# Kernel optimization log

Hardware: AMD Instinct MI355X
Metric: run time of the kernel (lower is better)

The kernel has to match this reference:

```python
import jax, jax.numpy as jnp
import numpy as np

DIM = 256
N_PATCHES = 2048
N_HEADS = 8
BATCH = 2


def setup_inputs() -> dict:
    key = jax.random.key(0)
    ks = jax.random.split(key, 8)
    d = DIM
    s = d ** -0.5
    return {
        "x": jax.random.normal(ks[0], (BATCH, N_PATCHES, d), dtype=jnp.float32),
        # weights stored (in_features, out_features) so y = x @ W + b
        "W_qk": jax.random.normal(ks[1], (d, 2 * d), dtype=jnp.float32) * s,
        "W_v": jax.random.normal(ks[2], (d, d), dtype=jnp.float32) * s,
        "W_proj": jax.random.normal(ks[3], (d, d), dtype=jnp.float32) * s,
        "b_proj": jnp.zeros((d,), dtype=jnp.float32),
        "W_pos": jax.random.normal(ks[4], (2, N_HEADS), dtype=jnp.float32) * 0.5,
        "b_pos": jnp.zeros((N_HEADS,), dtype=jnp.float32),
        "gating": jnp.ones((N_HEADS,), dtype=jnp.float32),
    }


def reference(x, W_qk, W_v, W_proj, b_proj, W_pos, b_pos, gating):
    B, N, C = x.shape
    H = gating.shape[0]
    Dh = C // H
    scale = Dh ** -0.5

    # content attention: q @ k^T softmax
    qk = (x @ W_qk).reshape(B, N, 2, H, Dh)
    q = jnp.transpose(qk[:, :, 0], (0, 2, 1, 3))  # [B,H,N,Dh]
    k = jnp.transpose(qk[:, :, 1], (0, 2, 1, 3))
    patch_score = jax.nn.softmax(jnp.einsum("bhnd,bhmd->bhnm", q, k) * scale, axis=-1)

    # positional attention from relative indices (d, |d|) -> per-head score
    idx = jnp.arange(N, dtype=jnp.float32)
    rel = idx[:, None] - idx[None, :]                      # [N,N]
    rel_feat = jnp.stack([rel, jnp.abs(rel)], axis=-1)     # [N,N,2]
    pos = rel_feat @ W_pos + b_pos                         # [N,N,H]
    pos_score = jax.nn.softmax(jnp.transpose(pos, (2, 0, 1)), axis=-1)  # [H,N,N]

    g = jax.nn.sigmoid(gating)[None, :, None, None]        # [1,H,1,1]
    attn = (1.0 - g) * patch_score + g * pos_score[None]   # [B,H,N,N]
    attn = attn / jnp.sum(attn, axis=-1, keepdims=True)

    v = jnp.transpose((x @ W_v).reshape(B, N, H, Dh), (0, 2, 1, 3))  # [B,H,N,Dh]
    out = jnp.einsum("bhnm,bhmd->bhnd", attn, v)
    out = jnp.transpose(out, (0, 2, 1, 3)).reshape(B, N, C)
    return out @ W_proj + b_proj
```

## Files before the change

### kernel.cpp

```cpp
#include <hip/hip_runtime.h>
#include <hip/hip_bf16.h>

#define DIM 256
#define NP 2048
#define NH 8
#define BATCH 2
#define DH 32

typedef __attribute__((ext_vector_type(8))) short bshort8;
typedef __attribute__((ext_vector_type(4))) short bshort4;
typedef __attribute__((ext_vector_type(4))) float f32x4;

#define LOG2E 1.44269504f
#define QSCALE (0.17677669529663687f * LOG2E)

union U16B { uint4 u; bshort8 s8; __hip_bfloat16 h[8]; };
union U8B  { uint2 u; bshort4 s4; __hip_bfloat16 h[4]; };

__device__ __forceinline__ float fexp2(float x) { return __builtin_amdgcn_exp2f(x); }
__device__ __forceinline__ unsigned packbf(float hi, float lo) {
    return __builtin_amdgcn_perm(__float_as_uint(hi), __float_as_uint(lo), 0x07060302u);
}

__device__ __forceinline__ int lds_addr(int row, int colg) {
    return row * 256 + (((colg ^ (row & 7)) & 31) << 3);
}

__global__ __launch_bounds__(256) void prep_kernel(
    const float* __restrict__ Wqk,
    const float* __restrict__ Wv,
    const float* __restrict__ Wproj,
    __hip_bfloat16* __restrict__ WT) {
    const int t = threadIdx.x;
    const int blk = blockIdx.x;
    __shared__ float ts[64][65];
    const int ct = blk >> 2, k0 = (blk & 3) * 64;
    const int c0 = ct * 64;
    const float* src; int ldw, cs0; float scl = 1.0f;
    if (ct < 8)       { src = Wqk;   ldw = 512; cs0 = c0;      if (ct < 4) scl = QSCALE; }
    else if (ct < 12) { src = Wv;    ldw = 256; cs0 = c0 - 512; }
    else              { src = Wproj; ldw = 256; cs0 = c0 - 768; }
    const int cc = t & 63, tq = t >> 6;
#pragma unroll
    for (int j = 0; j < 16; j++) {
        int kk = tq * 16 + j;
        ts[kk][cc] = src[(size_t)(k0 + kk) * ldw + cs0 + cc];
    }
    __syncthreads();
    const int kk2 = t & 63;
#pragma unroll
    for (int j = 0; j < 16; j++) {
        int cc2 = tq * 16 + j;
        WT[(size_t)(c0 + cc2) * 256 + k0 + kk2] = __float2bfloat16(ts[kk2][cc2] * scl);
    }
}

__global__ __launch_bounds__(256) void qkv_mfma(
    const float* __restrict__ x,
    const __hip_bfloat16* __restrict__ WT,
    __hip_bfloat16* __restrict__ q,
    __hip_bfloat16* __restrict__ k,
    __hip_bfloat16* __restrict__ vF) {
    __shared__ __align__(16) __hip_bfloat16 As[64 * 256];
    __shared__ __align__(16) __hip_bfloat16 Bs[64 * 256];
    const int t = threadIdx.x, lane = t & 63, wvid = t >> 6;
    const int l15 = lane & 15, l4 = lane >> 4;
    const int m0 = blockIdx.x * 64;
    const int nb0 = blockIdx.y * 64;

#pragma unroll
    for (int j = 0; j < 8; j++) {
        const int flat = j * 2048 + t * 8;
        const int row = flat >> 8, colg = (flat >> 3) & 31;
        float4 f0 = *(const float4*)(x + (size_t)m0 * 256 + flat);
        float4 f1 = *(const float4*)(x + (size_t)m0 * 256 + flat + 4);
        U16B a;
        a.h[0] = __float2bfloat16(f0.x); a.h[1] = __float2bfloat16(f0.y);
        a.h[2] = __float2bfloat16(f0.z); a.h[3] = __float2bfloat16(f0.w);
        a.h[4] = __float2bfloat16(f1.x); a.h[5] = __float2bfloat16(f1.y);
        a.h[6] = __float2bfloat16(f1.z); a.h[7] = __float2bfloat16(f1.w);
        *(uint4*)&As[lds_addr(row, colg)] = a.u;
        *(uint4*)&Bs[lds_addr(row, colg)] = *(const uint4*)(WT + (size_t)nb0 * 256 + flat);
    }
    __syncthreads();

    f32x4 acc[4] = {{0.f,0.f,0.f,0.f},{0.f,0.f,0.f,0.f},{0.f,0.f,0.f,0.f},{0.f,0.f,0.f,0.f}};
#pragma unroll
    for (int kk = 0; kk < 8; kk++) {
        const int colg = kk * 4 + l4;
        U16B bw; bw.u = *(const uint4*)&Bs[lds_addr(wvid * 16 + l15, colg)];
#pragma unroll
        for (int mt = 0; mt < 4; mt++) {
            U16B ax; ax.u = *(const uint4*)&As[lds_addr(mt * 16 + l15, colg)];
            acc[mt] = __builtin_amdgcn_mfma_f32_16x16x32_bf16(ax.s8, bw.s8, acc[mt], 0, 0, 0);
        }
    }

    if (nb0 < 512) {
        __syncthreads();
        __hip_bfloat16* Tr = As;
#pragma unroll
        for (int mt = 0; mt < 4; mt++)
#pragma unroll
            for (int r = 0; r < 4; r++)
                Tr[(mt * 16 + l4 * 4 + r) * 72 + wvid * 16 + l15] = __float2bfloat16(acc[mt][r]);
        __syncthreads();
        const int hh = t >> 7, row = (t >> 1) & 63, part = t & 1;
        const bool isq = (nb0 < 256);
        const int cc = (isq ? nb0 : nb0 - 256) + hh * 32;
        const int hOut = cc >> 5;
        const int tok = m0 + row;
        const int b = tok >> 11, n = tok & (NP - 1);
        __hip_bfloat16* dst = (isq ? q : k) + ((size_t)(b * NH + hOut) * NP + n) * DH + part * 16;
        uint4 w0 = *(const uint4*)&Tr[row * 72 + hh * 32 + part * 16];
        uint4 w1 = *(const uint4*)&Tr[row * 72 + hh * 32 + part * 16 + 8];
        *(uint4*)dst = w0;
        *(uint4*)(dst + 8) = w1;
    } else {
        const int cbase = (nb0 - 512) + wvid * 16;
        const int h = cbase >> 5;
        const int vh = (cbase >> 4) & 1;
        const int b = m0 >> 11;
#pragma unroll
        for (int mt = 0; mt < 4; mt++) {
            const int kt = ((m0 & (NP - 1)) >> 4) + mt;
            U8B vv;
#pragma unroll
            for (int r = 0; r < 4; r++) vv.h[r] = __float2bfloat16(acc[mt][r]);
            *(uint2*)(vF + ((((size_t)((b * NH + h) * 128 + kt)) * 2 + vh) * 64 + lane) * 4) = vv.u;
        }
    }
}

__global__ __launch_bounds__(512, 4) void attn_kernel(
    const __hip_bfloat16* __restrict__ qg,
    const __hip_bfloat16* __restrict__ kg,
    const __hip_bfloat16* __restrict__ vF,
    const float* __restrict__ Wpos,
    const float* __restrict__ bpos,
    const float* __restrict__ gating,
    __hip_bfloat16* __restrict__ ao) {
    __shared__ __align__(16) __hip_bfloat16 Kt[2][2][64][40];
    __shared__ __align__(16) __hip_bfloat16 Vf[2][2][2048];
    __shared__ float cmb[4][2][32][16];
    __shared__ float cls[4][2][16];

    const int t = threadIdx.x;
    const int lane = t & 63, wvid = t >> 6;
    const int l15 = lane & 15, l4 = lane >> 4;
    const int qt = wvid & 3, kh = wvid >> 2;
    const int bh = blockIdx.x >> 5, qb = blockIdx.x & 31;
    const int h = bh & (NH - 1), b = bh >> 3;
    const int q0 = qb * 64 + qt * 16;
    const int myq = q0 + l15;

    const int st_ = t & 255;
    const int kstart = kh * 1024;
    const __hip_bfloat16* kptr = kg + (size_t)bh * NP * DH + (size_t)(kstart + (st_ >> 2)) * DH + (st_ & 3) * 8;
    const __hip_bfloat16* vptr = vF + (size_t)bh * 65536 + (size_t)kstart * 32 + st_ * 8;

    uint4 kreg = *(const uint4*)kptr;
    uint4 vreg = *(const uint4*)vptr;
    *(uint4*)&Kt[kh][0][st_ >> 2][(st_ & 3) * 8] = kreg;
    *(uint4*)&Vf[kh][0][st_ * 8] = vreg;

    const float w0 = Wpos[h] * LOG2E;
    const float w1 = Wpos[NH + h] * LOG2E;
    const float g = 1.0f / (1.0f + __expf(-gating[h]));
    const float nf = (float)myq;
    const float pmax = fmaxf(0.f, fmaxf((w0 + w1) * nf, (w1 - w0) * (2047.0f - nf)));
    const float npmax = -pmax;
    const float rA = fexp2(-(w0 + w1));
    const float rB = fexp2(w1 - w0);

    U16B qv;
    qv.u = *(const uint4*)(qg + ((size_t)bh * NP + myq) * DH + l4 * 8);

    __syncthreads();

    f32x4 os0 = {0.f,0.f,0.f,0.f}, os1 = {0.f,0.f,0.f,0.f};
    f32x4 op0 = {0.f,0.f,0.f,0.f}, op1 = {0.f,0.f,0.f,0.f};
    float ls = 0.f, lp = 0.f;

    for (int it = 0; it < 16; ++it) {
        const int cur = it & 1, nxt = cur ^ 1;

        if (it < 15) {
            kreg = *(const uint4*)(kptr + (size_t)(it + 1) * 64 * DH);
            vreg = *(const uint4*)(vptr + (size_t)(it + 1) * 2048);
        }

        f32x4 st4[4];
#pragma unroll
        for (int kt = 0; kt < 4; kt++) {
            U16B kf; kf.u = *(const uint4*)&Kt[kh][cur][kt * 16 + l15][l4 * 8];
            st4[kt] = __builtin_amdgcn_mfma_f32_16x16x32_bf16(
                kf.s8, qv.s8, (f32x4){0.f,0.f,0.f,0.f}, 0, 0, 0);
        }

        U8B vfr[8];
#pragma unroll
        for (int vh = 0; vh < 2; vh++)
#pragma unroll
            for (int ktl = 0; ktl < 4; ktl++)
                vfr[vh * 4 + ktl].u = *(const uint2*)&Vf[kh][cur][((ktl * 2 + vh) * 64 + lane) * 4];

        const int kb0 = kstart + it * 64;
#pragma unroll
        for (int kt = 0; kt < 4; kt++) {
            float es0 = fexp2(st4[kt][0]), es1 = fexp2(st4[kt][1]);
            float es2 = fexp2(st4[kt][2]), es3 = fexp2(st4[kt][3]);
            ls += (es0 + es1) + (es2 + es3);
            const float d0 = nf - (float)(kb0 + kt * 16 + l4 * 4);
            float ep0 = fexp2(fmaf(w1, fabsf(d0), fmaf(w0, d0, npmax)));
            float ep1 = ep0 * ((d0 >= 1.f) ? rA : rB);
            float ep2 = ep1 * ((d0 >= 2.f) ? rA : rB);
            float ep3 = ep2 * ((d0 >= 3.f) ? rA : rB);
            lp += (ep0 + ep1) + (ep2 + ep3);
            U8B pc, pp;
            pc.u.x = packbf(es1, es0); pc.u.y = packbf(es3, es2);
            pp.u.x = packbf(ep1, ep0); pp.u.y = packbf(ep3, ep2);
            os0 = __builtin_amdgcn_mfma_f32_16x16x16bf16_1k(vfr[kt].s4,     pc.s4, os0, 0, 0, 0);
            os1 = __builtin_amdgcn_mfma_f32_16x16x16bf16_1k(vfr[4 + kt].s4, pc.s4, os1, 0, 0, 0);
            op0 = __builtin_amdgcn_mfma_f32_16x16x16bf16_1k(vfr[kt].s4,     pp.s4, op0, 0, 0, 0);
            op1 = __builtin_amdgcn_mfma_f32_16x16x16bf16_1k(vfr[4 + kt].s4, pp.s4, op1, 0, 0, 0);
        }

        if (it < 15) {
            *(uint4*)&Kt[kh][nxt][st_ >> 2][(st_ & 3) * 8] = kreg;
            *(uint4*)&Vf[kh][nxt][st_ * 8] = vreg;
        }
        __syncthreads();
    }

    ls += __shfl_xor(ls, 16, 64); ls += __shfl_xor(ls, 32, 64);
    lp += __shfl_xor(lp, 16, 64); lp += __shfl_xor(lp, 32, 64);

    if (kh == 1) {
#pragma unroll
        for (int r = 0; r < 4; r++) {
            cmb[qt][0][l4 * 4 + r][l15]      = os0[r];
            cmb[qt][0][16 + l4 * 4 + r][l15] = os1[r];
            cmb[qt][1][l4 * 4 + r][l15]      = op0[r];
            cmb[qt][1][16 + l4 * 4 + r][l15] = op1[r];
        }
        if (l4 == 0) { cls[qt][0][l15] = ls; cls[qt][1][l15] = lp; }
    }
    __syncthreads();
    if (kh == 0) {
        ls += cls[qt][0][l15]; lp += cls[qt][1][l15];
        const float cs = (1.0f - g) / ls;
        const float cp = g / lp;
        const size_t orow = ((size_t)b * NP + myq) * DIM + h * DH;
        U8B o0, o1;
#pragma unroll
        for (int r = 0; r < 4; r++) {
            o0.h[r] = __float2bfloat16(cs * (os0[r] + cmb[qt][0][l4 * 4 + r][l15]) +
                                       cp * (op0[r] + cmb[qt][1][l4 * 4 + r][l15]));
            o1.h[r] = __float2bfloat16(cs * (os1[r] + cmb[qt][0][16 + l4 * 4 + r][l15]) +
                                       cp * (op1[r] + cmb[qt][1][16 + l4 * 4 + r][l15]));
        }
        *(uint2*)(ao + orow + l4 * 4)      = o0.u;
        *(uint2*)(ao + orow + 16 + l4 * 4) = o1.u;
    }
}

__global__ __launch_bounds__(256) void proj_mfma(
    const __hip_bfloat16* __restrict__ ao,
    const __hip_bfloat16* __restrict__ WT,
    const float* __restrict__ bias,
    float* __restrict__ out) {
    __shared__ __align__(16) __hip_bfloat16 As[64 * 256];
    __shared__ __align__(16) __hip_bfloat16 Bs[64 * 256];
    const int t = threadIdx.x, lane = t & 63, wvid = t >> 6;
    const int l15 = lane & 15, l4 = lane >> 4;
    const int m0 = blockIdx.x * 64;
    const int nb0 = blockIdx.y * 64;
    const int nc = nb0 + wvid * 16 + l15;

#pragma unroll
    for (int j = 0; j < 8; j++) {
        const int flat = j * 2048 + t * 8;
        const int row = flat >> 8, colg = (flat >> 3) & 31;
        *(uint4*)&As[lds_addr(row, colg)] = *(const uint4*)(ao + (size_t)m0 * 256 + flat);
        *(uint4*)&Bs[lds_addr(row, colg)] = *(const uint4*)(WT + (size_t)(768 + nb0) * 256 + flat);
    }
    __syncthreads();

    f32x4 acc[4] = {{0.f,0.f,0.f,0.f},{0.f,0.f,0.f,0.f},{0.f,0.f,0.f,0.f},{0.f,0.f,0.f,0.f}};
#pragma unroll
    for (int kk = 0; kk < 8; kk++) {
        const int colg = kk * 4 + l4;
        U16B bw; bw.u = *(const uint4*)&Bs[lds_addr(wvid * 16 + l15, colg)];
#pragma unroll
        for (int mt = 0; mt < 4; mt++) {
            U16B ax; ax.u = *(const uint4*)&As[lds_addr(mt * 16 + l15, colg)];
            acc[mt] = __builtin_amdgcn_mfma_f32_16x16x32_bf16(ax.s8, bw.s8, acc[mt], 0, 0, 0);
        }
    }

    const float bb = bias[nc];
    __syncthreads();
    float* Trf = (float*)As;
#pragma unroll
    for (int mt = 0; mt < 4; mt++)
#pragma unroll
        for (int r = 0; r < 4; r++)
            Trf[(mt * 16 + l4 * 4 + r) * 68 + wvid * 16 + l15] = acc[mt][r] + bb;
    __syncthreads();
    const int row = t >> 2, seg = t & 3;
    float4 v0 = *(const float4*)&Trf[row * 68 + seg * 16];
    float4 v1 = *(const float4*)&Trf[row * 68 + seg * 16 + 4];
    float4 v2 = *(const float4*)&Trf[row * 68 + seg * 16 + 8];
    float4 v3 = *(const float4*)&Trf[row * 68 + seg * 16 + 12];
    float* dst = out + (size_t)(m0 + row) * 256 + nb0 + seg * 16;
    *(float4*)dst = v0;
    *(float4*)(dst + 4) = v1;
    *(float4*)(dst + 8) = v2;
    *(float4*)(dst + 12) = v3;
}

extern "C" void kernel_launch(void* const* d_in, const int* in_sizes, int n_in,
                              void* d_out, int out_size, void* d_ws, size_t ws_size,
                              hipStream_t stream) {
    const float* x      = (const float*)d_in[0];
    const float* Wqk    = (const float*)d_in[1];
    const float* Wv     = (const float*)d_in[2];
    const float* Wproj  = (const float*)d_in[3];
    const float* bproj  = (const float*)d_in[4];
    const float* Wpos   = (const float*)d_in[5];
    const float* bpos   = (const float*)d_in[6];
    const float* gating = (const float*)d_in[7];
    float* out = (float*)d_out;

    const size_t nElem = (size_t)BATCH * NP * DIM;
    char* w = (char*)d_ws;
    __hip_bfloat16* WT = (__hip_bfloat16*)w;
    __hip_bfloat16* q  = WT + 262144;
    __hip_bfloat16* k  = q + nElem;
    __hip_bfloat16* vF = k + nElem;
    __hip_bfloat16* ao = vF + nElem;

    prep_kernel<<<64, 256, 0, stream>>>(Wqk, Wv, Wproj, WT);
    qkv_mfma<<<dim3(64, 12), 256, 0, stream>>>(x, WT, q, k, vF);
    attn_kernel<<<BATCH * NH * (NP / 64), 512, 0, stream>>>(q, k, vF, Wpos, bpos, gating, ao);
    proj_mfma<<<dim3(64, 4), 256, 0, stream>>>(ao, WT, bproj, out);
}
```

Measured before the change: 109.1 us.

## Drop split-K in attention kernel, use 256-thread blocks looping over all keys

The attention kernel no longer splits the key range across two wave groups inside a 512-thread block. Each 256-thread block now walks all 2048 keys in 32 double-buffered iterations, and the LDS cross-group combine plus its extra barrier are gone. This halves shared memory per block and removes the reduction epilogue. The cost is half the waves per block with the same grid size (512 blocks), which lowers parallelism and latency hiding, and a serial loop twice as long.

```diff
diff --git a/kernel.cpp b/kernel.cpp
--- a/kernel.cpp
+++ b/kernel.cpp
@@ -132,7 +132,7 @@
     }
 }
 
-__global__ __launch_bounds__(512, 4) void attn_kernel(
+__global__ __launch_bounds__(256, 4) void attn_kernel(
     const __hip_bfloat16* __restrict__ qg,
     const __hip_bfloat16* __restrict__ kg,
     const __hip_bfloat16* __restrict__ vF,
@@ -140,29 +140,23 @@
     const float* __restrict__ bpos,
     const float* __restrict__ gating,
     __hip_bfloat16* __restrict__ ao) {
-    __shared__ __align__(16) __hip_bfloat16 Kt[2][2][64][40];
-    __shared__ __align__(16) __hip_bfloat16 Vf[2][2][2048];
-    __shared__ float cmb[4][2][32][16];
-    __shared__ float cls[4][2][16];
+    __shared__ __align__(16) __hip_bfloat16 Kt[2][64][40];
+    __shared__ __align__(16) __hip_bfloat16 Vf[2][2048];
 
     const int t = threadIdx.x;
-    const int lane = t & 63, wvid = t >> 6;
+    const int lane = t & 63, qt = t >> 6;
     const int l15 = lane & 15, l4 = lane >> 4;
-    const int qt = wvid & 3, kh = wvid >> 2;
     const int bh = blockIdx.x >> 5, qb = blockIdx.x & 31;
     const int h = bh & (NH - 1), b = bh >> 3;
-    const int q0 = qb * 64 + qt * 16;
-    const int myq = q0 + l15;
-
-    const int st_ = t & 255;
-    const int kstart = kh * 1024;
-    const __hip_bfloat16* kptr = kg + (size_t)bh * NP * DH + (size_t)(kstart + (st_ >> 2)) * DH + (st_ & 3) * 8;
-    const __hip_bfloat16* vptr = vF + (size_t)bh * 65536 + (size_t)kstart * 32 + st_ * 8;
+    const int myq = qb * 64 + qt * 16 + l15;
+
+    const __hip_bfloat16* kptr = kg + (size_t)bh * NP * DH + (size_t)(t >> 2) * DH + (t & 3) * 8;
+    const __hip_bfloat16* vptr = vF + (size_t)bh * 65536 + t * 8;
 
     uint4 kreg = *(const uint4*)kptr;
     uint4 vreg = *(const uint4*)vptr;
-    *(uint4*)&Kt[kh][0][st_ >> 2][(st_ & 3) * 8] = kreg;
-    *(uint4*)&Vf[kh][0][st_ * 8] = vreg;
+    *(uint4*)&Kt[0][t >> 2][(t & 3) * 8] = kreg;
+    *(uint4*)&Vf[0][t * 8] = vreg;
 
     const float w0 = Wpos[h] * LOG2E;
     const float w1 = Wpos[NH + h] * LOG2E;
@@ -182,10 +176,10 @@
     f32x4 op0 = {0.f,0.f,0.f,0.f}, op1 = {0.f,0.f,0.f,0.f};
     float ls = 0.f, lp = 0.f;
 
-    for (int it = 0; it < 16; ++it) {
+    for (int it = 0; it < 32; ++it) {
         const int cur = it & 1, nxt = cur ^ 1;
 
-        if (it < 15) {
+        if (it < 31) {
             kreg = *(const uint4*)(kptr + (size_t)(it + 1) * 64 * DH);
             vreg = *(const uint4*)(vptr + (size_t)(it + 1) * 2048);
         }
@@ -193,7 +187,7 @@
         f32x4 st4[4];
 #pragma unroll
         for (int kt = 0; kt < 4; kt++) {
-            U16B kf; kf.u = *(const uint4*)&Kt[kh][cur][kt * 16 + l15][l4 * 8];
+            U16B kf; kf.u = *(const uint4*)&Kt[cur][kt * 16 + l15][l4 * 8];
             st4[kt] = __builtin_amdgcn_mfma_f32_16x16x32_bf16(
                 kf.s8, qv.s8, (f32x4){0.f,0.f,0.f,0.f}, 0, 0, 0);
         }
@@ -203,9 +197,9 @@
         for (int vh = 0; vh < 2; vh++)
 #pragma unroll
             for (int ktl = 0; ktl < 4; ktl++)
-                vfr[vh * 4 + ktl].u = *(const uint2*)&Vf[kh][cur][((ktl * 2 + vh) * 64 + lane) * 4];
-
-        const int kb0 = kstart + it * 64;
+                vfr[vh * 4 + ktl].u = *(const uint2*)&Vf[cur][((ktl * 2 + vh) * 64 + lane) * 4];
+
+        const int kb0 = it * 64;
 #pragma unroll
         for (int kt = 0; kt < 4; kt++) {
             float es0 = fexp2(st4[kt][0]), es1 = fexp2(st4[kt][1]);
@@ -226,43 +220,27 @@
             op1 = __builtin_amdgcn_mfma_f32_16x16x16bf16_1k(vfr[4 + kt].s4, pp.s4, op1, 0, 0, 0);
         }
 
-        if (it < 15) {
-            *(uint4*)&Kt[kh][nxt][st_ >> 2][(st_ & 3) * 8] = kreg;
-            *(uint4*)&Vf[kh][nxt][st_ * 8] = vreg;
+        if (it < 31) {
+            *(uint4*)&Kt[nxt][t >> 2][(t & 3) * 8] = kreg;
+            *(uint4*)&Vf[nxt][t * 8] = vreg;
         }
         __syncthreads();
     }
 
     ls += __shfl_xor(ls, 16, 64); ls += __shfl_xor(ls, 32, 64);
     lp += __shfl_xor(lp, 16, 64); lp += __shfl_xor(lp, 32, 64);
-
-    if (kh == 1) {
-#pragma unroll
-        for (int r = 0; r < 4; r++) {
-            cmb[qt][0][l4 * 4 + r][l15]      = os0[r];
-            cmb[qt][0][16 + l4 * 4 + r][l15] = os1[r];
-            cmb[qt][1][l4 * 4 + r][l15]      = op0[r];
-            cmb[qt][1][16 + l4 * 4 + r][l15] = op1[r];
-        }
-        if (l4 == 0) { cls[qt][0][l15] = ls; cls[qt][1][l15] = lp; }
-    }
-    __syncthreads();
-    if (kh == 0) {
-        ls += cls[qt][0][l15]; lp += cls[qt][1][l15];
-        const float cs = (1.0f - g) / ls;
-        const float cp = g / lp;
-        const size_t orow = ((size_t)b * NP + myq) * DIM + h * DH;
-        U8B o0, o1;
-#pragma unroll
-        for (int r = 0; r < 4; r++) {
-            o0.h[r] = __float2bfloat16(cs * (os0[r] + cmb[qt][0][l4 * 4 + r][l15]) +
-                                       cp * (op0[r] + cmb[qt][1][l4 * 4 + r][l15]));
-            o1.h[r] = __float2bfloat16(cs * (os1[r] + cmb[qt][0][16 + l4 * 4 + r][l15]) +
-                                       cp * (op1[r] + cmb[qt][1][16 + l4 * 4 + r][l15]));
-        }
-        *(uint2*)(ao + orow + l4 * 4)      = o0.u;
-        *(uint2*)(ao + orow + 16 + l4 * 4) = o1.u;
-    }
+    const float cs = (1.0f - g) / ls;
+    const float cp = g / lp;
+
+    const size_t orow = ((size_t)b * NP + myq) * DIM + h * DH;
+    U8B o0, o1;
+#pragma unroll
+    for (int r = 0; r < 4; r++) {
+        o0.h[r] = __float2bfloat16(cs * os0[r] + cp * op0[r]);
+        o1.h[r] = __float2bfloat16(cs * os1[r] + cp * op1[r]);
+    }
+    *(uint2*)(ao + orow + l4 * 4)      = o0.u;
+    *(uint2*)(ao + orow + 16 + l4 * 4) = o1.u;
 }
 
 __global__ __launch_bounds__(256) void proj_mfma(
@@ -343,6 +321,6 @@
 
     prep_kernel<<<64, 256, 0, stream>>>(Wqk, Wv, Wproj, WT);
     qkv_mfma<<<dim3(64, 12), 256, 0, stream>>>(x, WT, q, k, vF);
-    attn_kernel<<<BATCH * NH * (NP / 64), 512, 0, stream>>>(q, k, vF, Wpos, bpos, gating, ao);
+    attn_kernel<<<BATCH * NH * (NP / 64), 256, 0, stream>>>(q, k, vF, Wpos, bpos, gating, ao);
     proj_mfma<<<dim3(64, 4), 256, 0, stream>>>(ao, WT, bproj, out);
 }
```

Measured after the change: 110.9 us. No clear change (+1.6%).
